# Performance work log

Measured on AMD Instinct MI355X. Metric: run time of the kernel, lower is better.

## Reference

```python
import math
import jax, jax.numpy as jnp
import numpy as np

N, C, T, V = 256, 128, 64, 25
OUT, H = 128, 4
D = OUT // H  # 32
MAX_LEN = 64
KSIZE = 9
EPS = 1e-5
NEG = -1e9


def setup_inputs() -> dict:
    key = jax.random.key(0)
    ks = jax.random.split(key, 20)
    std = 0.02
    return {
        "x": jax.random.normal(ks[0], (N, C, T, V), jnp.float32),
        # BatchNorm (eval mode) on input
        "bn_gamma": 1.0 + 0.1 * jax.random.normal(ks[1], (C,), jnp.float32),
        "bn_beta": 0.1 * jax.random.normal(ks[2], (C,), jnp.float32),
        "bn_mean": 0.1 * jax.random.normal(ks[3], (C,), jnp.float32),
        "bn_var": jax.random.uniform(ks[4], (C,), jnp.float32, 0.5, 1.5),
        # 1x1 convs (qkv_kernel=1)
        "qk_w": std * jax.random.normal(ks[5], (2 * OUT, C), jnp.float32),
        "qk_b": std * jax.random.normal(ks[6], (2 * OUT,), jnp.float32),
        "v_w": std * jax.random.normal(ks[7], (OUT, C), jnp.float32),
        "v_b": std * jax.random.normal(ks[8], (OUT,), jnp.float32),
        "logit_scale": jnp.full((H, 1, 1), math.log(math.sqrt(D)), jnp.float32),
        "rel_pos_bias": std * jax.random.normal(ks[9], (H, 2 * MAX_LEN - 1), jnp.float32),
        "proj_w": std * jax.random.normal(ks[10], (OUT, OUT), jnp.float32),
        "proj_b": std * jax.random.normal(ks[11], (OUT,), jnp.float32),
        # output BatchNorm (eval mode)
        "bno_gamma": 1.0 + 0.1 * jax.random.normal(ks[12], (OUT,), jnp.float32),
        "bno_beta": 0.1 * jax.random.normal(ks[13], (OUT,), jnp.float32),
        "bno_mean": 0.1 * jax.random.normal(ks[14], (OUT,), jnp.float32),
        "bno_var": jax.random.uniform(ks[15], (OUT,), jnp.float32, 0.5, 1.5),
    }


def _bn(x, gamma, beta, mean, var):
    # eval-mode BatchNorm2d over channel dim of (N, C, T, V)
    inv = gamma / jnp.sqrt(var + EPS)
    return (x - mean[:, None, None]) * inv[:, None, None] + beta[:, None, None]


def reference(x, bn_gamma, bn_beta, bn_mean, bn_var, qk_w, qk_b, v_w, v_b,
              logit_scale, rel_pos_bias, proj_w, proj_b,
              bno_gamma, bno_beta, bno_mean, bno_var):
    n, c, t, v = x.shape
    x_in = x
    xb = _bn(x, bn_gamma, bn_beta, bn_mean, bn_var)

    # 1x1 conv qk: (n, 2*OUT, t, v) -> split into q, k of shape (n, v, h, t, d)
    qk = jnp.einsum('nctv,oc->notv', xb, qk_w) + qk_b[:, None, None]
    qk = qk.reshape(n, 2, H, D, t, v).transpose(1, 0, 5, 2, 4, 3)  # (2, n, v, h, t, d)
    q, k = qk[0], qk[1]
    val = (jnp.einsum('nctv,oc->notv', xb, v_w) + v_b[:, None, None])
    val = val.reshape(n, H, D, t, v).transpose(0, 4, 1, 3, 2)  # (n, v, h, t, d)

    # cosine-sim attention: L2-normalize q, k; learned per-head temperature
    scale = jnp.exp(jnp.minimum(logit_scale, math.log(100.0)))  # (h,1,1)
    q = q / jnp.maximum(jnp.linalg.norm(q, axis=-1, keepdims=True), 1e-12) * scale
    k = k / jnp.maximum(jnp.linalg.norm(k, axis=-1, keepdims=True), 1e-12)

    # SDPA applies an extra 1/sqrt(d) scale by default
    scores = jnp.einsum('nvhid,nvhjd->nvhij', q, k) / math.sqrt(D)

    coords = jnp.arange(t)
    rel_idx = coords[None, :] - coords[:, None] + (MAX_LEN - 1)  # (t, t)
    bias = rel_pos_bias[:, rel_idx]  # (h, t, t)
    local = jnp.abs(coords[:, None] - coords[None, :]) <= KSIZE // 2  # (t, t)

    scores = jnp.where(local[None, None, None], scores + bias[None, None], NEG)
    attn = jax.nn.softmax(scores, axis=-1)
    out = jnp.einsum('nvhij,nvhjd->nvhid', attn, val)  # (n, v, h, t, d)
    out = out.transpose(0, 2, 4, 3, 1).reshape(n, OUT, t, v)

    out = jnp.einsum('nctv,oc->notv', out, proj_w) + proj_b[:, None, None] + x_in
    # stride=1 -> pool is identity; ffn_ratio=0 -> no FFN; dropout=0
    out = _bn(out, bno_gamma, bno_beta, bno_mean, bno_var)
    return out
```

## Files before the change

### kernel.cpp

```cpp
#include <hip/hip_runtime.h>
#include <hip/hip_bf16.h>

typedef __attribute__((ext_vector_type(8))) short bf16x8;
typedef __attribute__((ext_vector_type(4))) float f32x4;

static __device__ __forceinline__ unsigned short f2bf(float f){
  __hip_bfloat16 h = __float2bfloat16(f);
  return __builtin_bit_cast(unsigned short, h);
}
static __device__ __forceinline__ unsigned int pk2(float a, float b){
  return (unsigned int)f2bf(a) | ((unsigned int)f2bf(b) << 16);
}
static __device__ __forceinline__ float bf2f(unsigned short h){
  return __uint_as_float(((unsigned int)h) << 16);
}
static __device__ __forceinline__ f32x4 mfma16(bf16x8 a, bf16x8 b, f32x4 c){
  return __builtin_amdgcn_mfma_f32_16x16x32_bf16(a, b, c, 0, 0, 0);
}

__global__ void prep_kernel(
    const float* __restrict__ bn_g, const float* __restrict__ bn_b,
    const float* __restrict__ bn_m, const float* __restrict__ bn_v,
    const float* __restrict__ qk_w, const float* __restrict__ qk_b,
    const float* __restrict__ v_w,  const float* __restrict__ v_b,
    const float* __restrict__ ls,   const float* __restrict__ proj_w,
    const float* __restrict__ proj_b,
    const float* __restrict__ bo_g, const float* __restrict__ bo_b,
    const float* __restrict__ bo_m, const float* __restrict__ bo_v,
    unsigned short* __restrict__ Wqkv, unsigned short* __restrict__ Wp,
    float* __restrict__ bqf, float* __restrict__ bpf,
    float* __restrict__ rsf, float* __restrict__ shf)
{
  int g = blockIdx.x * 256 + threadIdx.x;
  if (g < 384){
    const float* wr = (g < 256) ? (qk_w + g * 128) : (v_w + (g - 256) * 128);
    float acc = (g < 256) ? qk_b[g] : v_b[g - 256];
    for (int c = 0; c < 128; c++){
      float inv = bn_g[c] * rsqrtf(bn_v[c] + 1e-5f);
      float sh  = bn_b[c] - bn_m[c] * inv;
      float wv  = wr[c];
      Wqkv[g * 128 + c] = f2bf(wv * inv);
      acc += wv * sh;
    }
    bqf[g] = acc;
  } else if (g < 512){
    int o = g - 384;
    float invo = bo_g[o] * rsqrtf(bo_v[o] + 1e-5f);
    for (int c = 0; c < 128; c++)
      Wp[o * 128 + c] = f2bf(proj_w[o * 128 + c] * invo);
    bpf[o] = (proj_b[o] - bo_m[o]) * invo + bo_b[o];
    rsf[o] = invo;
    if (o < 4)
      shf[o] = expf(fminf(ls[o], 4.6051701859880914f)) * 0.17677669529663687f;
  }
}

__global__ __launch_bounds__(256) void pack_x(const float* __restrict__ x,
                                              unsigned short* __restrict__ xb)
{
  __shared__ __align__(16) unsigned short tile[200][136];
  int n = blockIdx.x >> 3;
  int slab = blockIdx.x & 7;
  int t0 = slab * 8;
  int tid = threadIdx.x;
  const float* xn = x + (long)n * 204800 + (long)t0 * 25;
  #pragma unroll 5
  for (int k = 0; k < 25; k++){
    int idx = tid + k * 256;
    int c  = idx / 50;
    int r4 = idx - c * 50;
    float4 f = *((const float4*)(xn + (long)c * 1600 + r4 * 4));
    tile[r4*4+0][c] = f2bf(f.x);
    tile[r4*4+1][c] = f2bf(f.y);
    tile[r4*4+2][c] = f2bf(f.z);
    tile[r4*4+3][c] = f2bf(f.w);
  }
  __syncthreads();
  for (int k = 0; k < 13; k++){
    int idx = tid + k * 256;
    if (idx < 3200){
      int r  = idx >> 4;
      int u  = idx & 15;
      int lt = r / 25;
      int vv = r - lt * 25;
      int c0 = (u ^ lt) * 8;
      uint4 d = *((const uint4*)&tile[r][c0]);
      *((uint4*)(xb + ((long)(n * 25 + vv) * 64 + t0 + lt) * 128 + u * 8)) = d;
    }
  }
}

__global__ __launch_bounds__(256) void unpack_out(const unsigned short* __restrict__ ob,
                                                  float* __restrict__ out)
{
  __shared__ __align__(16) unsigned short tile[200][136];
  int n = blockIdx.x >> 3;
  int slab = blockIdx.x & 7;
  int t0 = slab * 8;
  int tid = threadIdx.x;
  for (int k = 0; k < 13; k++){
    int idx = tid + k * 256;
    if (idx < 3200){
      int r  = idx >> 4;
      int u  = idx & 15;
      int lt = r / 25;
      int vv = r - lt * 25;
      uint4 d = *((const uint4*)(ob + ((long)(n * 25 + vv) * 64 + t0 + lt) * 128 + u * 8));
      int c0 = (u ^ lt) * 8;
      *((uint4*)&tile[r][c0]) = d;
    }
  }
  __syncthreads();
  float* on = out + (long)n * 204800 + (long)t0 * 25;
  #pragma unroll 5
  for (int k = 0; k < 25; k++){
    int idx = tid + k * 256;
    int c  = idx / 50;
    int r4 = idx - c * 50;
    float4 f;
    f.x = bf2f(tile[r4*4+0][c]);
    f.y = bf2f(tile[r4*4+1][c]);
    f.z = bf2f(tile[r4*4+2][c]);
    f.w = bf2f(tile[r4*4+3][c]);
    *((float4*)(on + (long)c * 1600 + r4 * 4)) = f;
  }
}

#define B_RA    0
#define B_RB    16384
#define B_BQ    49152
#define B_BP    50688
#define B_RS    51200
#define B_SH    51712
#define B_BIAS  51728
#define B_TOTAL 53760

__global__ __launch_bounds__(256, 3) void fused_compute(
    const unsigned short* __restrict__ xb,
    const unsigned short* __restrict__ Wqkv,
    const unsigned short* __restrict__ Wp,
    const float* __restrict__ bqf,
    const float* __restrict__ bpf,
    const float* __restrict__ rsf,
    const float* __restrict__ shf,
    const float* __restrict__ relb,
    unsigned short* __restrict__ ob)
{
  __shared__ __align__(16) char smem[B_TOTAL];
  char* ra = smem + B_RA;
  float* c_bq   = (float*)(smem + B_BQ);
  float* c_bp   = (float*)(smem + B_BP);
  float* c_rs   = (float*)(smem + B_RS);
  float* c_sh   = (float*)(smem + B_SH);
  float* c_bias = (float*)(smem + B_BIAS);

  int bid = blockIdx.x;
  int swz = (bid & 7) * 800 + (bid >> 3);
  long tileoff = (long)swz * 8192;
  int tid  = threadIdx.x;
  int lane = tid & 63;
  int w    = tid >> 6;
  int h    = w;
  int l4   = lane >> 4;
  int l15  = lane & 15;

  char* qkh = smem + B_RB + h * 8192;

  for (int i = tid; i < 384; i += 256) c_bq[i] = bqf[i];
  if (tid < 128){ c_bp[tid] = bpf[tid]; c_rs[tid] = rsf[tid]; }
  if (tid < 4) c_sh[tid] = shf[tid];
  for (int i = tid; i < 508; i += 256) c_bias[i] = relb[i];
  {
    const uint4* src = (const uint4*)(xb + tileoff);
    uint4* dst = (uint4*)ra;
    #pragma unroll
    for (int i = 0; i < 4; i++) dst[tid + i * 256] = src[tid + i * 256];
  }
  __syncthreads();

  const f32x4 zero4 = {0.f, 0.f, 0.f, 0.f};
  uint2 resid[2][4];

  {
    int rb[4] = {32*h, 32*h + 16, 128 + 32*h, 128 + 32*h + 16};
    f32x4 acc[4][4];
    #pragma unroll
    for (int m = 0; m < 4; m++)
      #pragma unroll
      for (int nt = 0; nt < 4; nt++) acc[m][nt] = zero4;
    #pragma unroll
    for (int ks = 0; ks < 4; ks++){
      int ko = ks * 32 + l4 * 8;
      bf16x8 a[4], b[4];
      #pragma unroll
      for (int m = 0; m < 4; m++)
        a[m] = *((const bf16x8*)(Wqkv + (rb[m] + l15) * 128 + ko));
      #pragma unroll
      for (int nt = 0; nt < 4; nt++){
        int row = nt * 16 + l15;
        b[nt] = *((const bf16x8*)(ra + row * 256 + ((ko * 2) ^ ((row & 7) << 4))));
      }
      #pragma unroll
      for (int m = 0; m < 4; m++)
        #pragma unroll
        for (int nt = 0; nt < 4; nt++)
          acc[m][nt] = mfma16(a[m], b[nt], acc[m][nt]);
    }
    #pragma unroll
    for (int m = 0; m < 4; m++)
      #pragma unroll
      for (int nt = 0; nt < 4; nt++)
        #pragma unroll
        for (int r = 0; r < 4; r++)
          acc[m][nt][r] += c_bq[rb[m] + l4 * 4 + r];

    #pragma unroll
    for (int nt = 0; nt < 4; nt++){
      float ssq = 0.f, ssk = 0.f;
      #pragma unroll
      for (int r = 0; r < 4; r++){
        ssq += acc[0][nt][r] * acc[0][nt][r] + acc[1][nt][r] * acc[1][nt][r];
        ssk += acc[2][nt][r] * acc[2][nt][r] + acc[3][nt][r] * acc[3][nt][r];
      }
      ssq += __shfl_xor(ssq, 16); ssq += __shfl_xor(ssq, 32);
      ssk += __shfl_xor(ssk, 16); ssk += __shfl_xor(ssk, 32);
      float scq = c_sh[h] / fmaxf(sqrtf(ssq), 1e-12f);
      float sck = 1.0f   / fmaxf(sqrtf(ssk), 1e-12f);
      int row = nt * 16 + l15;
      #pragma unroll
      for (int m = 0; m < 2; m++){
        uint2 p;
        p.x = pk2(acc[m][nt][0] * scq, acc[m][nt][1] * scq);
        p.y = pk2(acc[m][nt][2] * scq, acc[m][nt][3] * scq);
        *((uint2*)(qkh + row * 128 + ((m * 32 + l4 * 8) ^ ((row & 7) << 4)))) = p;
      }
      #pragma unroll
      for (int m = 2; m < 4; m++){
        uint2 p;
        p.x = pk2(acc[m][nt][0] * sck, acc[m][nt][1] * sck);
        p.y = pk2(acc[m][nt][2] * sck, acc[m][nt][3] * sck);
        *((uint2*)(qkh + row * 128 + ((64 + (m - 2) * 32 + l4 * 8) ^ ((row & 7) << 4)))) = p;
      }
    }
  }

  {
    int rb4 = 256 + 32 * h, rb5 = 256 + 32 * h + 16;
    f32x4 accv[2][4];
    #pragma unroll
    for (int m = 0; m < 2; m++)
      #pragma unroll
      for (int nt = 0; nt < 4; nt++) accv[m][nt] = zero4;
    #pragma unroll
    for (int ks = 0; ks < 4; ks++){
      int ko = ks * 32 + l4 * 8;
      bf16x8 a0 = *((const bf16x8*)(Wqkv + (rb4 + l15) * 128 + ko));
      bf16x8 a1 = *((const bf16x8*)(Wqkv + (rb5 + l15) * 128 + ko));
      #pragma unroll
      for (int nt = 0; nt < 4; nt++){
        int row = nt * 16 + l15;
        bf16x8 b = *((const bf16x8*)(ra + row * 256 + ((ko * 2) ^ ((row & 7) << 4))));
        accv[0][nt] = mfma16(a0, b, accv[0][nt]);
        accv[1][nt] = mfma16(a1, b, accv[1][nt]);
      }
    }
    #pragma unroll
    for (int mt = 0; mt < 2; mt++)
      #pragma unroll
      for (int nt = 0; nt < 4; nt++){
        int o0 = w * 32 + mt * 16 + l4 * 4;
        int t2 = nt * 16 + l15;
        resid[mt][nt] = *((const uint2*)(ra + t2 * 256 + ((o0 * 2) ^ ((t2 & 7) << 4))));
      }
    __syncthreads();

    #pragma unroll
    for (int m = 0; m < 2; m++)
      #pragma unroll
      for (int nt = 0; nt < 4; nt++)
        #pragma unroll
        for (int r = 0; r < 4; r++){
          int d = h * 32 + m * 16 + l4 * 4 + r;
          float vv = accv[m][nt][r] + c_bq[256 + h * 32 + m * 16 + l4 * 4 + r];
          *((unsigned short*)(ra + d * 128 + ((((nt * 16 + l15) * 2)) ^ ((d & 7) << 4)))) = f2bf(vv);
        }
  }
  __builtin_amdgcn_sched_barrier(0);

  bf16x8 kf[4], qf[4];
  {
    #pragma unroll
    for (int jt = 0; jt < 4; jt++){
      int row = jt * 16 + l15;
      kf[jt] = *((const bf16x8*)(qkh + row * 128 + ((64 + l4 * 16) ^ ((row & 7) << 4))));
    }
    #pragma unroll
    for (int it = 0; it < 4; it++){
      int row = it * 16 + l15;
      qf[it] = *((const bf16x8*)(qkh + row * 128 + ((l4 * 16) ^ ((row & 7) << 4))));
    }
  }
  __builtin_amdgcn_sched_barrier(0);

  {
    f32x4 sAcc[4][4];
    #pragma unroll
    for (int jt = 0; jt < 4; jt++)
      #pragma unroll
      for (int it = 0; it < 4; it++) sAcc[jt][it] = zero4;
    #pragma unroll
    for (int jt = 0; jt < 4; jt++)
      #pragma unroll
      for (int it = 0; it < 4; it++)
        sAcc[jt][it] = mfma16(kf[jt], qf[it], sAcc[jt][it]);

    #pragma unroll
    for (int it = 0; it < 4; it++){
      int i = it * 16 + l15;
      float sv[16];
      float mx = -1e30f;
      #pragma unroll
      for (int jt = 0; jt < 4; jt++){
        #pragma unroll
        for (int r = 0; r < 4; r++){
          int j = jt * 16 + l4 * 4 + r;
          int rel = j - i;
          float s;
          if (rel < -4 || rel > 4) s = -1e9f;
          else s = sAcc[jt][it][r] + c_bias[h * 127 + rel + 63];
          sv[jt * 4 + r] = s;
          mx = fmaxf(mx, s);
        }
      }
      mx = fmaxf(mx, __shfl_xor(mx, 16));
      mx = fmaxf(mx, __shfl_xor(mx, 32));
      float sum = 0.f;
      #pragma unroll
      for (int k2 = 0; k2 < 16; k2++){
        float p = __expf(sv[k2] - mx);
        sv[k2] = p; sum += p;
      }
      sum += __shfl_xor(sum, 16);
      sum += __shfl_xor(sum, 32);
      float rs = 1.0f / sum;
      #pragma unroll
      for (int jt = 0; jt < 4; jt++){
        uint2 p;
        p.x = pk2(sv[jt*4+0] * rs, sv[jt*4+1] * rs);
        p.y = pk2(sv[jt*4+2] * rs, sv[jt*4+3] * rs);
        *((uint2*)(qkh + i * 128 + ((jt * 32 + l4 * 8) ^ ((i & 7) << 4)))) = p;
      }
    }
  }
  __builtin_amdgcn_sched_barrier(0);

  bf16x8 av[2][2], bv2[4][2];
  {
    #pragma unroll
    for (int mt = 0; mt < 2; mt++)
      #pragma unroll
      for (int ks2 = 0; ks2 < 2; ks2++){
        int row = h * 32 + mt * 16 + l15;
        av[mt][ks2] = *((const bf16x8*)(ra + row * 128 + ((ks2 * 64 + l4 * 16) ^ ((row & 7) << 4))));
      }
    #pragma unroll
    for (int it = 0; it < 4; it++)
      #pragma unroll
      for (int ks2 = 0; ks2 < 2; ks2++){
        int row = it * 16 + l15;
        bv2[it][ks2] = *((const bf16x8*)(qkh + row * 128 + ((ks2 * 64 + l4 * 16) ^ ((row & 7) << 4))));
      }
  }
  __syncthreads();

  unsigned short* ao = (unsigned short*)(smem + B_RB);
  {
    f32x4 pAcc[2][4];
    #pragma unroll
    for (int mt = 0; mt < 2; mt++)
      #pragma unroll
      for (int it = 0; it < 4; it++) pAcc[mt][it] = zero4;
    #pragma unroll
    for (int mt = 0; mt < 2; mt++)
      #pragma unroll
      for (int it = 0; it < 4; it++)
        #pragma unroll
        for (int ks2 = 0; ks2 < 2; ks2++)
          pAcc[mt][it] = mfma16(av[mt][ks2], bv2[it][ks2], pAcc[mt][it]);
    #pragma unroll
    for (int mt = 0; mt < 2; mt++)
      #pragma unroll
      for (int it = 0; it < 4; it++){
        int d0 = mt * 16 + l4 * 4;
        int i  = it * 16 + l15;
        uint2 p;
        p.x = pk2(pAcc[mt][it][0], pAcc[mt][it][1]);
        p.y = pk2(pAcc[mt][it][2], pAcc[mt][it][3]);
        *((uint2*)&ao[i * 136 + h * 32 + d0]) = p;
      }
  }
  __syncthreads();

  {
    f32x4 acc2[2][4];
    #pragma unroll
    for (int mt = 0; mt < 2; mt++)
      #pragma unroll
      for (int nt = 0; nt < 4; nt++) acc2[mt][nt] = zero4;
    #pragma unroll
    for (int ks = 0; ks < 4; ks++){
      int ko = ks * 32 + l4 * 8;
      bf16x8 a2[2], b2[4];
      #pragma unroll
      for (int mt = 0; mt < 2; mt++)
        a2[mt] = *((const bf16x8*)(Wp + (w * 32 + mt * 16 + l15) * 128 + ko));
      #pragma unroll
      for (int nt = 0; nt < 4; nt++)
        b2[nt] = *((const bf16x8*)&ao[(nt * 16 + l15) * 136 + ko]);
      #pragma unroll
      for (int mt = 0; mt < 2; mt++)
        #pragma unroll
        for (int nt = 0; nt < 4; nt++)
          acc2[mt][nt] = mfma16(a2[mt], b2[nt], acc2[mt][nt]);
    }
    #pragma unroll
    for (int mt = 0; mt < 2; mt++)
      #pragma unroll
      for (int nt = 0; nt < 4; nt++){
        int o0 = w * 32 + mt * 16 + l4 * 4;
        int t2 = nt * 16 + l15;
        uint2 rd = resid[mt][nt];
        float r0 = bf2f((unsigned short)(rd.x & 0xFFFFu));
        float r1f = bf2f((unsigned short)(rd.x >> 16));
        float r2 = bf2f((unsigned short)(rd.y & 0xFFFFu));
        float r3 = bf2f((unsigned short)(rd.y >> 16));
        uint2 p;
        p.x = pk2(acc2[mt][nt][0] + c_bp[o0+0] + r0 * c_rs[o0+0],
                  acc2[mt][nt][1] + c_bp[o0+1] + r1f * c_rs[o0+1]);
        p.y = pk2(acc2[mt][nt][2] + c_bp[o0+2] + r2 * c_rs[o0+2],
                  acc2[mt][nt][3] + c_bp[o0+3] + r3 * c_rs[o0+3]);
        *((uint2*)(ra + t2 * 256 + ((o0 * 2) ^ ((t2 & 7) << 4)))) = p;
      }
  }
  __syncthreads();
  {
    const uint4* sxl = (const uint4*)ra;
    uint4* obt = (uint4*)(ob + tileoff);
    #pragma unroll
    for (int i = 0; i < 4; i++) obt[tid + i * 256] = sxl[tid + i * 256];
  }
}

#define F_X     0
#define F_RB    17408
#define F_VT    58368
#define F_BQ    76800
#define F_BP    78336
#define F_RS    78848
#define F_SH    79360
#define F_BIAS  79376
#define F_TOTAL 81408

__global__ __launch_bounds__(256, 2) void fused_scatter(
    const float* __restrict__ x,
    const unsigned short* __restrict__ Wqkv,
    const unsigned short* __restrict__ Wp,
    const float* __restrict__ bqf,
    const float* __restrict__ bpf,
    const float* __restrict__ rsf,
    const float* __restrict__ shf,
    const float* __restrict__ relb,
    float* __restrict__ out)
{
  __shared__ __align__(16) char smem[F_TOTAL];
  unsigned short* xl   = (unsigned short*)(smem + F_X);
  unsigned short* rbu  = (unsigned short*)(smem + F_RB);
  unsigned short* vT   = (unsigned short*)(smem + F_VT);
  float* c_bq   = (float*)(smem + F_BQ);
  float* c_bp   = (float*)(smem + F_BP);
  float* c_rs   = (float*)(smem + F_RS);
  float* c_sh   = (float*)(smem + F_SH);
  float* c_bias = (float*)(smem + F_BIAS);

  int bid = blockIdx.x;
  int swz = (bid & 7) * 800 + (bid >> 3);
  int n = swz / 25;
  int v = swz - n * 25;
  int tid  = threadIdx.x;
  int lane = tid & 63;
  int w    = tid >> 6;
  int l4   = lane >> 4;
  int l15  = lane & 15;

  for (int i = tid; i < 384; i += 256) c_bq[i] = bqf[i];
  if (tid < 128){ c_bp[tid] = bpf[tid]; c_rs[tid] = rsf[tid]; }
  if (tid < 4) c_sh[tid] = shf[tid];
  for (int i = tid; i < 508; i += 256) c_bias[i] = relb[i];

  {
    const float* xb2 = x + (long)n * 204800 + v;
    int t  = lane;
    int cg = w * 32;
    #pragma unroll
    for (int i = 0; i < 4; i++){
      unsigned int pk[4];
      #pragma unroll
      for (int e = 0; e < 4; e++){
        int c = cg + i * 8 + e * 2;
        pk[e] = pk2(xb2[(long)c * 1600 + t * 25], xb2[(long)(c + 1) * 1600 + t * 25]);
      }
      uint4 q4; q4.x = pk[0]; q4.y = pk[1]; q4.z = pk[2]; q4.w = pk[3];
      *((uint4*)&xl[t * 136 + cg + i * 8]) = q4;
    }
  }
  __syncthreads();

  const f32x4 zero4 = {0.f, 0.f, 0.f, 0.f};

  {
    f32x4 acc[6][4];
    #pragma unroll
    for (int m = 0; m < 6; m++)
      #pragma unroll
      for (int nt = 0; nt < 4; nt++) acc[m][nt] = zero4;
    int Mb = w * 96;
    #pragma unroll
    for (int ks = 0; ks < 4; ks++){
      int ko = ks * 32 + l4 * 8;
      bf16x8 a[6], b[4];
      #pragma unroll
      for (int m = 0; m < 6; m++)
        a[m] = *((const bf16x8*)(Wqkv + (Mb + m * 16 + l15) * 128 + ko));
      #pragma unroll
      for (int nt = 0; nt < 4; nt++)
        b[nt] = *((const bf16x8*)&xl[(nt * 16 + l15) * 136 + ko]);
      #pragma unroll
      for (int m = 0; m < 6; m++)
        #pragma unroll
        for (int nt = 0; nt < 4; nt++)
          acc[m][nt] = mfma16(a[m], b[nt], acc[m][nt]);
    }
    #pragma unroll
    for (int m = 0; m < 6; m++){
      #pragma unroll
      for (int nt = 0; nt < 4; nt++){
        #pragma unroll
        for (int r = 0; r < 4; r++){
          int o  = Mb + m * 16 + l4 * 4 + r;
          int t2 = nt * 16 + l15;
          unsigned short bv = f2bf(acc[m][nt][r] + c_bq[o]);
          if (o < 256){
            rbu[(((o >> 7) * 4 + ((o >> 5) & 3)) * 64 + t2) * 40 + (o & 31)] = bv;
          } else {
            vT[(o - 256) * 72 + t2] = bv;
          }
        }
      }
    }
  }
  __syncthreads();

  {
    #pragma unroll
    for (int rr = 0; rr < 2; rr++){
      int r = tid + rr * 256;
      unsigned short* row = &rbu[r * 40];
      uint4 u0 = *((uint4*)(row + 0));
      uint4 u1 = *((uint4*)(row + 8));
      uint4 u2 = *((uint4*)(row + 16));
      uint4 u3 = *((uint4*)(row + 24));
      unsigned int uu[16] = {u0.x,u0.y,u0.z,u0.w, u1.x,u1.y,u1.z,u1.w,
                             u2.x,u2.y,u2.z,u2.w, u3.x,u3.y,u3.z,u3.w};
      float vals[32];
      float ss = 0.f;
      #pragma unroll
      for (int k2 = 0; k2 < 16; k2++){
        float f0 = bf2f((unsigned short)(uu[k2] & 0xFFFFu));
        float f1 = bf2f((unsigned short)(uu[k2] >> 16));
        vals[2*k2] = f0; vals[2*k2+1] = f1;
        ss += f0 * f0 + f1 * f1;
      }
      float sc = 1.0f / fmaxf(sqrtf(ss), 1e-12f);
      if (r < 256) sc *= c_sh[(r >> 6) & 3];
      #pragma unroll
      for (int k2 = 0; k2 < 16; k2++)
        uu[k2] = pk2(vals[2*k2] * sc, vals[2*k2+1] * sc);
      u0.x=uu[0];u0.y=uu[1];u0.z=uu[2];u0.w=uu[3];
      u1.x=uu[4];u1.y=uu[5];u1.z=uu[6];u1.w=uu[7];
      u2.x=uu[8];u2.y=uu[9];u2.z=uu[10];u2.w=uu[11];
      u3.x=uu[12];u3.y=uu[13];u3.z=uu[14];u3.w=uu[15];
      *((uint4*)(row + 0))  = u0;
      *((uint4*)(row + 8))  = u1;
      *((uint4*)(row + 16)) = u2;
      *((uint4*)(row + 24)) = u3;
    }
  }
  __syncthreads();

  int h = w;
  bf16x8 kf[4], qf[4];
  {
    const unsigned short* kb = &rbu[(256 + h * 64) * 40];
    const unsigned short* qb = &rbu[(h * 64) * 40];
    int ko = l4 * 8;
    #pragma unroll
    for (int jt = 0; jt < 4; jt++)
      kf[jt] = *((const bf16x8*)(kb + (jt * 16 + l15) * 40 + ko));
    #pragma unroll
    for (int it = 0; it < 4; it++)
      qf[it] = *((const bf16x8*)(qb + (it * 16 + l15) * 40 + ko));
  }
  __syncthreads();

  unsigned short* attn = rbu + h * 4608;
  {
    f32x4 sAcc[4][4];
    #pragma unroll
    for (int jt = 0; jt < 4; jt++)
      #pragma unroll
      for (int it = 0; it < 4; it++) sAcc[jt][it] = zero4;
    #pragma unroll
    for (int jt = 0; jt < 4; jt++)
      #pragma unroll
      for (int it = 0; it < 4; it++)
        sAcc[jt][it] = mfma16(kf[jt], qf[it], sAcc[jt][it]);

    #pragma unroll
    for (int it = 0; it < 4; it++){
      int i = it * 16 + l15;
      float sv[16];
      float mx = -1e30f;
      #pragma unroll
      for (int jt = 0; jt < 4; jt++){
        #pragma unroll
        for (int r = 0; r < 4; r++){
          int j = jt * 16 + l4 * 4 + r;
          int rel = j - i;
          float s;
          if (rel < -4 || rel > 4) s = -1e9f;
          else s = sAcc[jt][it][r] + c_bias[h * 127 + rel + 63];
          sv[jt * 4 + r] = s;
          mx = fmaxf(mx, s);
        }
      }
      mx = fmaxf(mx, __shfl_xor(mx, 16));
      mx = fmaxf(mx, __shfl_xor(mx, 32));
      float sum = 0.f;
      #pragma unroll
      for (int k2 = 0; k2 < 16; k2++){
        float p = __expf(sv[k2] - mx);
        sv[k2] = p; sum += p;
      }
      sum += __shfl_xor(sum, 16);
      sum += __shfl_xor(sum, 32);
      float rs = 1.0f / sum;
      #pragma unroll
      for (int jt = 0; jt < 4; jt++)
        #pragma unroll
        for (int r = 0; r < 4; r++)
          attn[i * 72 + (jt * 16 + l4 * 4 + r)] = f2bf(sv[jt * 4 + r] * rs);
    }
  }

  bf16x8 av[2][2], bv2[4][2];
  {
    int ko = l4 * 8;
    #pragma unroll
    for (int mt = 0; mt < 2; mt++)
      #pragma unroll
      for (int ks2 = 0; ks2 < 2; ks2++)
        av[mt][ks2] = *((const bf16x8*)&vT[(h * 32 + mt * 16 + l15) * 72 + ks2 * 32 + ko]);
    #pragma unroll
    for (int it = 0; it < 4; it++)
      #pragma unroll
      for (int ks2 = 0; ks2 < 2; ks2++)
        bv2[it][ks2] = *((const bf16x8*)&attn[(it * 16 + l15) * 72 + ks2 * 32 + ko]);
  }
  __syncthreads();

  unsigned short* ao = rbu;
  {
    f32x4 pAcc[2][4];
    #pragma unroll
    for (int mt = 0; mt < 2; mt++)
      #pragma unroll
      for (int it = 0; it < 4; it++) pAcc[mt][it] = zero4;
    #pragma unroll
    for (int mt = 0; mt < 2; mt++)
      #pragma unroll
      for (int it = 0; it < 4; it++)
        #pragma unroll
        for (int ks2 = 0; ks2 < 2; ks2++)
          pAcc[mt][it] = mfma16(av[mt][ks2], bv2[it][ks2], pAcc[mt][it]);
    #pragma unroll
    for (int mt = 0; mt < 2; mt++)
      #pragma unroll
      for (int it = 0; it < 4; it++)
        #pragma unroll
        for (int r = 0; r < 4; r++){
          int d = mt * 16 + l4 * 4 + r;
          int i = it * 16 + l15;
          ao[i * 136 + h * 32 + d] = f2bf(pAcc[mt][it][r]);
        }
  }
  __syncthreads();

  {
    f32x4 acc2[2][4];
    #pragma unroll
    for (int mt = 0; mt < 2; mt++)
      #pragma unroll
      for (int nt = 0; nt < 4; nt++) acc2[mt][nt] = zero4;
    #pragma unroll
    for (int ks = 0; ks < 4; ks++){
      int ko = ks * 32 + l4 * 8;
      bf16x8 a2[2], b2[4];
      #pragma unroll
      for (int mt = 0; mt < 2; mt++)
        a2[mt] = *((const bf16x8*)(Wp + (w * 32 + mt * 16 + l15) * 128 + ko));
      #pragma unroll
      for (int nt = 0; nt < 4; nt++)
        b2[nt] = *((const bf16x8*)&ao[(nt * 16 + l15) * 136 + ko]);
      #pragma unroll
      for (int mt = 0; mt < 2; mt++)
        #pragma unroll
        for (int nt = 0; nt < 4; nt++)
          acc2[mt][nt] = mfma16(a2[mt], b2[nt], acc2[mt][nt]);
    }
    float* outp = out + (long)n * 204800 + v;
    #pragma unroll
    for (int mt = 0; mt < 2; mt++)
      #pragma unroll
      for (int nt = 0; nt < 4; nt++)
        #pragma unroll
        for (int r = 0; r < 4; r++){
          int o  = w * 32 + mt * 16 + l4 * 4 + r;
          int t2 = nt * 16 + l15;
          float val = acc2[mt][nt][r] + c_bp[o] + bf2f(xl[t2 * 136 + o]) * c_rs[o];
          outp[(long)o * 1600 + t2 * 25] = val;
        }
  }
}

extern "C" void kernel_launch(void* const* d_in, const int* in_sizes, int n_in,
                              void* d_out, int out_size, void* d_ws, size_t ws_size,
                              hipStream_t stream)
{
  const float* x     = (const float*)d_in[0];
  const float* bn_g  = (const float*)d_in[1];
  const float* bn_b  = (const float*)d_in[2];
  const float* bn_m  = (const float*)d_in[3];
  const float* bn_v  = (const float*)d_in[4];
  const float* qk_w  = (const float*)d_in[5];
  const float* qk_b  = (const float*)d_in[6];
  const float* v_w   = (const float*)d_in[7];
  const float* v_b   = (const float*)d_in[8];
  const float* ls    = (const float*)d_in[9];
  const float* relb  = (const float*)d_in[10];
  const float* pj_w  = (const float*)d_in[11];
  const float* pj_b  = (const float*)d_in[12];
  const float* bo_g  = (const float*)d_in[13];
  const float* bo_b  = (const float*)d_in[14];
  const float* bo_m  = (const float*)d_in[15];
  const float* bo_v  = (const float*)d_in[16];

  const size_t XB_BYTES = 104857600;
  const size_t NEED = 2 * XB_BYTES + 98304 + 32768 + 1536 + 512 + 512 + 16;

  char* ws = (char*)d_ws;
  size_t wbase = (ws_size >= NEED) ? (2 * XB_BYTES) : 0;

  unsigned short* Wqkv = (unsigned short*)(ws + wbase);
  unsigned short* Wp   = (unsigned short*)(ws + wbase + 98304);
  float* bqf = (float*)(ws + wbase + 131072);
  float* bpf = (float*)(ws + wbase + 132608);
  float* rsf = (float*)(ws + wbase + 133120);
  float* shf = (float*)(ws + wbase + 133632);

  hipLaunchKernelGGL(prep_kernel, dim3(2), dim3(256), 0, stream,
                     bn_g, bn_b, bn_m, bn_v, qk_w, qk_b, v_w, v_b, ls,
                     pj_w, pj_b, bo_g, bo_b, bo_m, bo_v,
                     Wqkv, Wp, bqf, bpf, rsf, shf);

  if (ws_size >= NEED){
    unsigned short* xb = (unsigned short*)(ws);
    unsigned short* ob = (unsigned short*)(ws + XB_BYTES);
    hipLaunchKernelGGL(pack_x, dim3(2048), dim3(256), 0, stream, x, xb);
    hipLaunchKernelGGL(fused_compute, dim3(6400), dim3(256), 0, stream,
                       xb, Wqkv, Wp, bqf, bpf, rsf, shf, relb, ob);
    hipLaunchKernelGGL(unpack_out, dim3(2048), dim3(256), 0, stream, ob, (float*)d_out);
  } else {
    hipLaunchKernelGGL(fused_scatter, dim3(6400), dim3(256), 0, stream,
                       x, Wqkv, Wp, bqf, bpf, rsf, shf, relb, (float*)d_out);
  }
}
```

Baseline: 317.4 us.

## Skip masked score tiles, drop softmax max pass, shrink pack/unpack tiles

The score MFMAs now run only for the tridiagonal band of 16x16 tiles that can fall inside the local window of ±4. Softmax drops the row-max reduction and exponentiates directly, relying on cosine-similarity scores being bounded. Separately, pack_x and unpack_out now process 4 time steps per block instead of 8, doubling the grid and halving LDS use, with an added row-based XOR swizzle to cut bank conflicts on the transposed LDS accesses. Dropping the max subtraction risks overflow if the logit scale were large, though here it is clamped.

```diff
diff --git a/kernel.cpp b/kernel.cpp
--- a/kernel.cpp
+++ b/kernel.cpp
@@ -58,33 +58,36 @@
 __global__ __launch_bounds__(256) void pack_x(const float* __restrict__ x,
                                               unsigned short* __restrict__ xb)
 {
-  __shared__ __align__(16) unsigned short tile[200][136];
-  int n = blockIdx.x >> 3;
-  int slab = blockIdx.x & 7;
-  int t0 = slab * 8;
+  __shared__ __align__(16) unsigned short tile[100][136];
+  int n = blockIdx.x >> 4;
+  int slab = blockIdx.x & 15;
+  int t0 = slab * 4;
   int tid = threadIdx.x;
   const float* xn = x + (long)n * 204800 + (long)t0 * 25;
-  #pragma unroll 5
-  for (int k = 0; k < 25; k++){
-    int idx = tid + k * 256;
-    int c  = idx / 50;
-    int r4 = idx - c * 50;
-    float4 f = *((const float4*)(xn + (long)c * 1600 + r4 * 4));
-    tile[r4*4+0][c] = f2bf(f.x);
-    tile[r4*4+1][c] = f2bf(f.y);
-    tile[r4*4+2][c] = f2bf(f.z);
-    tile[r4*4+3][c] = f2bf(f.w);
-  }
-  __syncthreads();
   for (int k = 0; k < 13; k++){
     int idx = tid + k * 256;
     if (idx < 3200){
+      int c  = idx / 25;
+      int r4 = idx - c * 25;
+      float4 f = *((const float4*)(xn + (long)c * 1600 + r4 * 4));
+      int r0 = r4 * 4;
+      tile[r0+0][c ^ (8*((r0+0)&7))] = f2bf(f.x);
+      tile[r0+1][c ^ (8*((r0+1)&7))] = f2bf(f.y);
+      tile[r0+2][c ^ (8*((r0+2)&7))] = f2bf(f.z);
+      tile[r0+3][c ^ (8*((r0+3)&7))] = f2bf(f.w);
+    }
+  }
+  __syncthreads();
+  for (int k = 0; k < 7; k++){
+    int idx = tid + k * 256;
+    if (idx < 1600){
       int r  = idx >> 4;
       int u  = idx & 15;
       int lt = r / 25;
       int vv = r - lt * 25;
-      int c0 = (u ^ lt) * 8;
-      uint4 d = *((const uint4*)&tile[r][c0]);
+      int t7 = (t0 & 4) + lt;
+      int c0 = (u ^ t7) * 8;
+      uint4 d = *((const uint4*)&tile[r][c0 ^ (8*(r&7))]);
       *((uint4*)(xb + ((long)(n * 25 + vv) * 64 + t0 + lt) * 128 + u * 8)) = d;
     }
   }
@@ -93,36 +96,39 @@
 __global__ __launch_bounds__(256) void unpack_out(const unsigned short* __restrict__ ob,
                                                   float* __restrict__ out)
 {
-  __shared__ __align__(16) unsigned short tile[200][136];
-  int n = blockIdx.x >> 3;
-  int slab = blockIdx.x & 7;
-  int t0 = slab * 8;
+  __shared__ __align__(16) unsigned short tile[100][136];
+  int n = blockIdx.x >> 4;
+  int slab = blockIdx.x & 15;
+  int t0 = slab * 4;
   int tid = threadIdx.x;
-  for (int k = 0; k < 13; k++){
+  for (int k = 0; k < 7; k++){
     int idx = tid + k * 256;
-    if (idx < 3200){
+    if (idx < 1600){
       int r  = idx >> 4;
       int u  = idx & 15;
       int lt = r / 25;
       int vv = r - lt * 25;
       uint4 d = *((const uint4*)(ob + ((long)(n * 25 + vv) * 64 + t0 + lt) * 128 + u * 8));
-      int c0 = (u ^ lt) * 8;
-      *((uint4*)&tile[r][c0]) = d;
+      int t7 = (t0 & 4) + lt;
+      int c0 = (u ^ t7) * 8;
+      *((uint4*)&tile[r][c0 ^ (8*(r&7))]) = d;
     }
   }
   __syncthreads();
   float* on = out + (long)n * 204800 + (long)t0 * 25;
-  #pragma unroll 5
-  for (int k = 0; k < 25; k++){
+  for (int k = 0; k < 13; k++){
     int idx = tid + k * 256;
-    int c  = idx / 50;
-    int r4 = idx - c * 50;
-    float4 f;
-    f.x = bf2f(tile[r4*4+0][c]);
-    f.y = bf2f(tile[r4*4+1][c]);
-    f.z = bf2f(tile[r4*4+2][c]);
-    f.w = bf2f(tile[r4*4+3][c]);
-    *((float4*)(on + (long)c * 1600 + r4 * 4)) = f;
+    if (idx < 3200){
+      int c  = idx / 25;
+      int r4 = idx - c * 25;
+      int r0 = r4 * 4;
+      float4 f;
+      f.x = bf2f(tile[r0+0][c ^ (8*((r0+0)&7))]);
+      f.y = bf2f(tile[r0+1][c ^ (8*((r0+1)&7))]);
+      f.z = bf2f(tile[r0+2][c ^ (8*((r0+2)&7))]);
+      f.w = bf2f(tile[r0+3][c ^ (8*((r0+3)&7))]);
+      *((float4*)(on + (long)c * 1600 + r4 * 4)) = f;
+    }
   }
 }
 
@@ -312,33 +318,27 @@
     for (int jt = 0; jt < 4; jt++)
       #pragma unroll
       for (int it = 0; it < 4; it++)
-        sAcc[jt][it] = mfma16(kf[jt], qf[it], sAcc[jt][it]);
+        if (jt <= it + 1 && it <= jt + 1)
+          sAcc[jt][it] = mfma16(kf[jt], qf[it], sAcc[jt][it]);
 
     #pragma unroll
     for (int it = 0; it < 4; it++){
       int i = it * 16 + l15;
       float sv[16];
-      float mx = -1e30f;
+      float sum = 0.f;
       #pragma unroll
       for (int jt = 0; jt < 4; jt++){
+        if (jt + 1 < it || jt > it + 1) continue;
         #pragma unroll
         for (int r = 0; r < 4; r++){
           int j = jt * 16 + l4 * 4 + r;
           int rel = j - i;
-          float s;
-          if (rel < -4 || rel > 4) s = -1e9f;
-          else s = sAcc[jt][it][r] + c_bias[h * 127 + rel + 63];
-          sv[jt * 4 + r] = s;
-          mx = fmaxf(mx, s);
+          float s = sAcc[jt][it][r] + c_bias[h * 127 + rel + 63];
+          bool inb = (rel >= -4) && (rel <= 4);
+          float p = inb ? __expf(s) : 0.f;
+          sv[jt * 4 + r] = p;
+          sum += p;
         }
-      }
-      mx = fmaxf(mx, __shfl_xor(mx, 16));
-      mx = fmaxf(mx, __shfl_xor(mx, 32));
-      float sum = 0.f;
-      #pragma unroll
-      for (int k2 = 0; k2 < 16; k2++){
-        float p = __expf(sv[k2] - mx);
-        sv[k2] = p; sum += p;
       }
       sum += __shfl_xor(sum, 16);
       sum += __shfl_xor(sum, 32);
@@ -346,8 +346,12 @@
       #pragma unroll
       for (int jt = 0; jt < 4; jt++){
         uint2 p;
-        p.x = pk2(sv[jt*4+0] * rs, sv[jt*4+1] * rs);
-        p.y = pk2(sv[jt*4+2] * rs, sv[jt*4+3] * rs);
+        if (jt + 1 < it || jt > it + 1){
+          p.x = 0u; p.y = 0u;
+        } else {
+          p.x = pk2(sv[jt*4+0] * rs, sv[jt*4+1] * rs);
+          p.y = pk2(sv[jt*4+2] * rs, sv[jt*4+3] * rs);
+        }
         *((uint2*)(qkh + i * 128 + ((jt * 32 + l4 * 8) ^ ((i & 7) << 4)))) = p;
       }
     }
@@ -785,10 +789,10 @@
   if (ws_size >= NEED){
     unsigned short* xb = (unsigned short*)(ws);
     unsigned short* ob = (unsigned short*)(ws + XB_BYTES);
-    hipLaunchKernelGGL(pack_x, dim3(2048), dim3(256), 0, stream, x, xb);
+    hipLaunchKernelGGL(pack_x, dim3(4096), dim3(256), 0, stream, x, xb);
     hipLaunchKernelGGL(fused_compute, dim3(6400), dim3(256), 0, stream,
                        xb, Wqkv, Wp, bqf, bpf, rsf, shf, relb, ob);
-    hipLaunchKernelGGL(unpack_out, dim3(2048), dim3(256), 0, stream, ob, (float*)d_out);
+    hipLaunchKernelGGL(unpack_out, dim3(4096), dim3(256), 0, stream, ob, (float*)d_out);
   } else {
     hipLaunchKernelGGL(fused_scatter, dim3(6400), dim3(256), 0, stream,
                        x, Wqkv, Wp, bqf, bpf, rsf, shf, relb, (float*)d_out);
```

Result: slower. 332.8 us (+4.8%).

## Skip out-of-band score tiles, drop softmax max pass, fold prep into pack_x

Applied to the files above, without the earlier changes.

The score MFMAs now run only on the tridiagonal 16x16 tiles that can hold in-band entries, and probabilities for far tiles are written as zeros. Softmax no longer subtracts the row max, since cosine-similarity scores are bounded by the clamped temperature. Weight preparation moves into the first two blocks of pack_x, removing one kernel launch. The risk is overflow if the scale ever exceeds its bound; in practice it is clamped, so exp stays finite.

```diff
diff --git a/kernel.cpp b/kernel.cpp
--- a/kernel.cpp
+++ b/kernel.cpp
@@ -16,6 +16,42 @@
 }
 static __device__ __forceinline__ f32x4 mfma16(bf16x8 a, bf16x8 b, f32x4 c){
   return __builtin_amdgcn_mfma_f32_16x16x32_bf16(a, b, c, 0, 0, 0);
+}
+
+static __device__ __forceinline__ void prep_body(int g,
+    const float* __restrict__ bn_g, const float* __restrict__ bn_b,
+    const float* __restrict__ bn_m, const float* __restrict__ bn_v,
+    const float* __restrict__ qk_w, const float* __restrict__ qk_b,
+    const float* __restrict__ v_w,  const float* __restrict__ v_b,
+    const float* __restrict__ ls,   const float* __restrict__ proj_w,
+    const float* __restrict__ proj_b,
+    const float* __restrict__ bo_g, const float* __restrict__ bo_b,
+    const float* __restrict__ bo_m, const float* __restrict__ bo_v,
+    unsigned short* __restrict__ Wqkv, unsigned short* __restrict__ Wp,
+    float* __restrict__ bqf, float* __restrict__ bpf,
+    float* __restrict__ rsf, float* __restrict__ shf)
+{
+  if (g < 384){
+    const float* wr = (g < 256) ? (qk_w + g * 128) : (v_w + (g - 256) * 128);
+    float acc = (g < 256) ? qk_b[g] : v_b[g - 256];
+    for (int c = 0; c < 128; c++){
+      float inv = bn_g[c] * rsqrtf(bn_v[c] + 1e-5f);
+      float sh  = bn_b[c] - bn_m[c] * inv;
+      float wv  = wr[c];
+      Wqkv[g * 128 + c] = f2bf(wv * inv);
+      acc += wv * sh;
+    }
+    bqf[g] = acc;
+  } else if (g < 512){
+    int o = g - 384;
+    float invo = bo_g[o] * rsqrtf(bo_v[o] + 1e-5f);
+    for (int c = 0; c < 128; c++)
+      Wp[o * 128 + c] = f2bf(proj_w[o * 128 + c] * invo);
+    bpf[o] = (proj_b[o] - bo_m[o]) * invo + bo_b[o];
+    rsf[o] = invo;
+    if (o < 4)
+      shf[o] = expf(fminf(ls[o], 4.6051701859880914f)) * 0.17677669529663687f;
+  }
 }
 
 __global__ void prep_kernel(
@@ -32,31 +68,23 @@
     float* __restrict__ rsf, float* __restrict__ shf)
 {
   int g = blockIdx.x * 256 + threadIdx.x;
-  if (g < 384){
-    const float* wr = (g < 256) ? (qk_w + g * 128) : (v_w + (g - 256) * 128);
-    float acc = (g < 256) ? qk_b[g] : v_b[g - 256];
-    for (int c = 0; c < 128; c++){
-      float inv = bn_g[c] * rsqrtf(bn_v[c] + 1e-5f);
-      float sh  = bn_b[c] - bn_m[c] * inv;
-      float wv  = wr[c];
-      Wqkv[g * 128 + c] = f2bf(wv * inv);
-      acc += wv * sh;
-    }
-    bqf[g] = acc;
-  } else if (g < 512){
-    int o = g - 384;
-    float invo = bo_g[o] * rsqrtf(bo_v[o] + 1e-5f);
-    for (int c = 0; c < 128; c++)
-      Wp[o * 128 + c] = f2bf(proj_w[o * 128 + c] * invo);
-    bpf[o] = (proj_b[o] - bo_m[o]) * invo + bo_b[o];
-    rsf[o] = invo;
-    if (o < 4)
-      shf[o] = expf(fminf(ls[o], 4.6051701859880914f)) * 0.17677669529663687f;
-  }
+  prep_body(g, bn_g, bn_b, bn_m, bn_v, qk_w, qk_b, v_w, v_b, ls,
+            proj_w, proj_b, bo_g, bo_b, bo_m, bo_v, Wqkv, Wp, bqf, bpf, rsf, shf);
 }
 
 __global__ __launch_bounds__(256) void pack_x(const float* __restrict__ x,
-                                              unsigned short* __restrict__ xb)
+    unsigned short* __restrict__ xb,
+    const float* __restrict__ bn_g, const float* __restrict__ bn_b,
+    const float* __restrict__ bn_m, const float* __restrict__ bn_v,
+    const float* __restrict__ qk_w, const float* __restrict__ qk_b,
+    const float* __restrict__ v_w,  const float* __restrict__ v_b,
+    const float* __restrict__ ls,   const float* __restrict__ proj_w,
+    const float* __restrict__ proj_b,
+    const float* __restrict__ bo_g, const float* __restrict__ bo_b,
+    const float* __restrict__ bo_m, const float* __restrict__ bo_v,
+    unsigned short* __restrict__ Wqkv, unsigned short* __restrict__ Wp,
+    float* __restrict__ bqf, float* __restrict__ bpf,
+    float* __restrict__ rsf, float* __restrict__ shf)
 {
   __shared__ __align__(16) unsigned short tile[200][136];
   int n = blockIdx.x >> 3;
@@ -87,6 +115,11 @@
       uint4 d = *((const uint4*)&tile[r][c0]);
       *((uint4*)(xb + ((long)(n * 25 + vv) * 64 + t0 + lt) * 128 + u * 8)) = d;
     }
+  }
+  if (blockIdx.x < 2){
+    int g = blockIdx.x * 256 + tid;
+    prep_body(g, bn_g, bn_b, bn_m, bn_v, qk_w, qk_b, v_w, v_b, ls,
+              proj_w, proj_b, bo_g, bo_b, bo_m, bo_v, Wqkv, Wp, bqf, bpf, rsf, shf);
   }
 }
 
@@ -312,33 +345,27 @@
     for (int jt = 0; jt < 4; jt++)
       #pragma unroll
       for (int it = 0; it < 4; it++)
-        sAcc[jt][it] = mfma16(kf[jt], qf[it], sAcc[jt][it]);
+        if (jt <= it + 1 && it <= jt + 1)
+          sAcc[jt][it] = mfma16(kf[jt], qf[it], sAcc[jt][it]);
 
     #pragma unroll
     for (int it = 0; it < 4; it++){
       int i = it * 16 + l15;
       float sv[16];
-      float mx = -1e30f;
+      float sum = 0.f;
       #pragma unroll
       for (int jt = 0; jt < 4; jt++){
+        if (jt + 1 < it || jt > it + 1) continue;
         #pragma unroll
         for (int r = 0; r < 4; r++){
           int j = jt * 16 + l4 * 4 + r;
           int rel = j - i;
-          float s;
-          if (rel < -4 || rel > 4) s = -1e9f;
-          else s = sAcc[jt][it][r] + c_bias[h * 127 + rel + 63];
-          sv[jt * 4 + r] = s;
-          mx = fmaxf(mx, s);
+          float s = sAcc[jt][it][r] + c_bias[h * 127 + rel + 63];
+          bool inb = (rel >= -4) && (rel <= 4);
+          float p = inb ? __expf(s) : 0.f;
+          sv[jt * 4 + r] = p;
+          sum += p;
         }
-      }
-      mx = fmaxf(mx, __shfl_xor(mx, 16));
-      mx = fmaxf(mx, __shfl_xor(mx, 32));
-      float sum = 0.f;
-      #pragma unroll
-      for (int k2 = 0; k2 < 16; k2++){
-        float p = __expf(sv[k2] - mx);
-        sv[k2] = p; sum += p;
       }
       sum += __shfl_xor(sum, 16);
       sum += __shfl_xor(sum, 32);
@@ -346,8 +373,12 @@
       #pragma unroll
       for (int jt = 0; jt < 4; jt++){
         uint2 p;
-        p.x = pk2(sv[jt*4+0] * rs, sv[jt*4+1] * rs);
-        p.y = pk2(sv[jt*4+2] * rs, sv[jt*4+3] * rs);
+        if (jt + 1 < it || jt > it + 1){
+          p.x = 0u; p.y = 0u;
+        } else {
+          p.x = pk2(sv[jt*4+0] * rs, sv[jt*4+1] * rs);
+          p.y = pk2(sv[jt*4+2] * rs, sv[jt*4+3] * rs);
+        }
         *((uint2*)(qkh + i * 128 + ((jt * 32 + l4 * 8) ^ ((i & 7) << 4)))) = p;
       }
     }
@@ -777,19 +808,21 @@
   float* rsf = (float*)(ws + wbase + 133120);
   float* shf = (float*)(ws + wbase + 133632);
 
-  hipLaunchKernelGGL(prep_kernel, dim3(2), dim3(256), 0, stream,
-                     bn_g, bn_b, bn_m, bn_v, qk_w, qk_b, v_w, v_b, ls,
-                     pj_w, pj_b, bo_g, bo_b, bo_m, bo_v,
-                     Wqkv, Wp, bqf, bpf, rsf, shf);
-
   if (ws_size >= NEED){
     unsigned short* xb = (unsigned short*)(ws);
     unsigned short* ob = (unsigned short*)(ws + XB_BYTES);
-    hipLaunchKernelGGL(pack_x, dim3(2048), dim3(256), 0, stream, x, xb);
+    hipLaunchKernelGGL(pack_x, dim3(2048), dim3(256), 0, stream, x, xb,
+                       bn_g, bn_b, bn_m, bn_v, qk_w, qk_b, v_w, v_b, ls,
+                       pj_w, pj_b, bo_g, bo_b, bo_m, bo_v,
+                       Wqkv, Wp, bqf, bpf, rsf, shf);
     hipLaunchKernelGGL(fused_compute, dim3(6400), dim3(256), 0, stream,
                        xb, Wqkv, Wp, bqf, bpf, rsf, shf, relb, ob);
     hipLaunchKernelGGL(unpack_out, dim3(2048), dim3(256), 0, stream, ob, (float*)d_out);
   } else {
+    hipLaunchKernelGGL(prep_kernel, dim3(2), dim3(256), 0, stream,
+                       bn_g, bn_b, bn_m, bn_v, qk_w, qk_b, v_w, v_b, ls,
+                       pj_w, pj_b, bo_g, bo_b, bo_m, bo_v,
+                       Wqkv, Wp, bqf, bpf, rsf, shf);
     hipLaunchKernelGGL(fused_scatter, dim3(6400), dim3(256), 0, stream,
                        x, Wqkv, Wp, bqf, bpf, rsf, shf, relb, (float*)d_out);
   }
```

New measurement: 298.7 us. -5.9%, faster.
